# Kernel optimization log

Measured on AMD Instinct MI355X. Metric: run time of the kernel, lower is better.

## Reference

```python
import jax, jax.numpy as jnp
import numpy as np

MLP_DIMS = [256, 128, 64, 32, 1]

def setup_inputs() -> dict:
    key = jax.random.key(0)
    ks = jax.random.split(key, 16)
    N, C, sp = 2, 256, 512
    inp = {
        'points': jax.random.normal(ks[0], (N, C, sp), dtype=jnp.float32),
        'heatMap': jax.random.uniform(ks[1], (N, sp, sp), dtype=jnp.float32),
        'mask': jnp.ones((N, sp, sp), dtype=jnp.float32),
        'positiveMask': jax.random.uniform(ks[2], (N, sp, sp), dtype=jnp.float32),
    }
    # MLP params: 256->128->64->32->1, Kaiming-ish scale
    for i, (din, dout) in enumerate(zip(MLP_DIMS[:-1], MLP_DIMS[1:])):
        inp[f'W{i}'] = jax.random.normal(ks[4 + i], (din, dout), dtype=jnp.float32) * (1.0 / np.sqrt(din))
        inp[f'b{i}'] = jnp.zeros((dout,), dtype=jnp.float32)
    return inp


def _mlp(x, Ws, bs):
    # Linear+ReLU cascade; final layer is a raw logit (no activation).
    n = len(Ws)
    for i, (W, b) in enumerate(zip(Ws, bs)):
        x = jnp.einsum('...i,io->...o', x, W) + b
        if i < n - 1:
            x = jax.nn.relu(x)
    return x


def _bce_with_logits(logits, targets):
    # stable elementwise BCE-with-logits, reduction='none'
    return jnp.maximum(logits, 0.0) - logits * targets + jnp.log1p(jnp.exp(-jnp.abs(logits)))


def reference(points, heatMap, mask, positiveMask, W0, b0, W1, b1, W2, b2, W3, b3):
    p = jnp.transpose(points, (0, 2, 1))          # (N, sp, C)
    X = p[:, :, None, :] + p[:, None, :, :]       # (N, sp, sp, C)
    pred = _mlp(X, [W0, W1, W2, W3], [b0, b1, b2, b3])[..., 0]  # (N, sp, sp)
    loss = _bce_with_logits(pred, heatMap) * mask * positiveMask
    loss = loss.sum() / positiveMask.sum()
    return (pred, loss)
```

## Files before the change

### kernel.cpp

```cpp
#include <hip/hip_runtime.h>
#include <hip/hip_bf16.h>
#include <stdint.h>

#define N_ 2
#define C_ 256
#define SP 512
#define H1 128
#define H2 64
#define H3 32
#define NTILE 1056
#define GRID 256

using f32x4 = __attribute__((ext_vector_type(4))) float;
using u32x4 = __attribute__((ext_vector_type(4))) unsigned int;
using s16x8 = __attribute__((ext_vector_type(8))) short;

__device__ __forceinline__ uint32_t f2bf_rne(float x) {
    uint32_t u = __builtin_bit_cast(uint32_t, x);
    return (u + 0x7FFFu + ((u >> 16) & 1u)) >> 16;
}
__device__ __forceinline__ float bf2f(uint32_t h) {
    return __builtin_bit_cast(float, h << 16);
}
__device__ __forceinline__ uint32_t pkbf(float a, float b) {
    __hip_bfloat162 h = __float22bfloat162_rn(make_float2(a, b));
    uint32_t r;
    __builtin_memcpy(&r, &h, 4);
    return r;
}
__device__ __forceinline__ uint16_t bf1(float a) {
    __hip_bfloat16 h = __float2bfloat16(a);
    uint16_t r;
    __builtin_memcpy(&r, &h, 2);
    return r;
}
__device__ __forceinline__ f32x4 ntload4(const float* p) {
    return __builtin_nontemporal_load((const f32x4*)p);
}

__device__ __forceinline__ void unrank_tile(int tau, int& n, int& iBase, int& jBase)
{
    int nn = (tau >= 528) ? 1 : 0;
    int u = tau - nn * 528;
    int bi = (int)((65.0f - sqrtf(4225.0f - 8.0f * (float)u)) * 0.5f);
    int s = bi * (65 - bi) / 2;
    while (s > u) { --bi; s = bi * (65 - bi) / 2; }
    while (u - s >= 32 - bi) { ++bi; s = bi * (65 - bi) / 2; }
    int bj = bi + (u - s);
    n = nn; iBase = bi * 16; jBase = bj * 16;
}

__global__ __launch_bounds__(512) void k_precompA(
    const float* __restrict__ points, const float* __restrict__ W0,
    const float* __restrict__ b0,
    const float* __restrict__ W1, const float* __restrict__ W2,
    float* __restrict__ A,
    short* __restrict__ W1Th, short* __restrict__ W2Th, short* __restrict__ W2Tl,
    float* __restrict__ accum)
{
    int t = threadIdx.x;
    if (blockIdx.x == 0 && t < 4) accum[t] = 0.0f;
    int k4 = t & 31;
    int team = t >> 5;
    int rloc = team & 3, cq = team >> 2;
    int row = blockIdx.x * 4 + rloc;
    int n = row >> 9, i = row & (SP - 1);
    const float* pb = points + (size_t)n * C_ * SP + i;
    f32x4 p0 = {0.f, 0.f, 0.f, 0.f}, p1 = {0.f, 0.f, 0.f, 0.f};
    int c0 = cq * 64;
#pragma unroll 8
    for (int c = c0; c < c0 + 64; c += 2) {
        float s0 = pb[(size_t)c * SP];
        float s1 = pb[(size_t)(c + 1) * SP];
        f32x4 w0v = *(const f32x4*)(W0 + c * H1 + k4 * 4);
        f32x4 w1v = *(const f32x4*)(W0 + (c + 1) * H1 + k4 * 4);
#pragma unroll
        for (int e = 0; e < 4; ++e) {
            p0[e] = fmaf(s0, w0v[e], p0[e]);
            p1[e] = fmaf(s1, w1v[e], p1[e]);
        }
    }
#pragma unroll
    for (int e = 0; e < 4; ++e) p0[e] += p1[e];
    __shared__ f32x4 part[16][32];
    part[team][k4] = p0;
    __syncthreads();
    int r2 = t >> 7, kk = t & 127;
    float s = 0.5f * b0[kk]
            + part[r2][kk >> 2][kk & 3] + part[r2 + 4][kk >> 2][kk & 3]
            + part[r2 + 8][kk >> 2][kk & 3] + part[r2 + 12][kk >> 2][kk & 3];
    A[(size_t)(blockIdx.x * 4 + r2) * H1 + kk] = s;

    int gid = blockIdx.x * 512 + t;
    int gstride = gridDim.x * 512;
    for (int idx = gid; idx < H2 * H1; idx += gstride) {
        int col = idx >> 7, k = idx & 127;
        int sidx = col * 128 + ((((k >> 3) ^ (col & 15)) << 3) | (k & 7));
        W1Th[sidx] = (short)f2bf_rne(W1[k * H2 + col]);
    }
    for (int idx = gid; idx < H3 * H2; idx += gstride) {
        int col = idx >> 6, k = idx & 63;
        float wv = W2[k * H3 + col];
        uint32_t h = f2bf_rne(wv);
        int sidx = col * 64 + ((((k >> 3) ^ (col & 7)) << 3) | (k & 7));
        W2Th[sidx] = (short)h;
        W2Tl[sidx] = (short)f2bf_rne(wv - bf2f(h));
    }
}

__global__ __launch_bounds__(512, 2) void k_main(
    const float* __restrict__ A,
    const short* __restrict__ wtab,
    const float* __restrict__ b1, const float* __restrict__ b2,
    const float* __restrict__ W3, const float* __restrict__ b3,
    const float* __restrict__ heat, const float* __restrict__ mask,
    const float* __restrict__ pos,
    float* __restrict__ pred, float* __restrict__ accum, float* __restrict__ loss)
{
    __shared__ __align__(16) char smem[32768 + 32768 + 16384 + 2176 + 64];
    int t = threadIdx.x;
    int bid = blockIdx.x;
    int l = t & 63, w = t >> 6;
    int lc = l & 15, kg = l >> 4;
    char* x2b = smem + 32768 + w * 4096;
    char* x3b = smem + 65536 + w * 2048;
    char* zbB = smem + 81920;
    float* rb = (float*)(smem + 81920 + 2176);

    const short* lw1h = wtab;
    const short* lw2h = wtab + 8192;
    const short* lw2l = wtab + 10240;

    int rST = t >> 5, segST = t & 31;

    s16x8 bw3;
    {
        f32x4 wa = *(const f32x4*)(W3 + kg * 8);
        f32x4 wb = *(const f32x4*)(W3 + kg * 8 + 4);
        u32x4 wp;
        wp[0] = pkbf(wa[0], wa[1]);
        wp[1] = pkbf(wa[2], wa[3]);
        wp[2] = pkbf(wb[0], wb[1]);
        wp[3] = pkbf(wb[2], wb[3]);
        bw3 = __builtin_bit_cast(s16x8, wp);
    }
    float b3v = b3[0];

    float num = 0.0f, den = 0.0f;

    {
        int n0, ib0, jb0; unrank_tile(bid, n0, ib0, jb0);
        const float* Ab = A + (size_t)n0 * SP * H1;
        f32x4 va = ntload4(Ab + (size_t)(ib0 + rST) * H1 + segST * 4);
        f32x4 vb = ntload4(Ab + (size_t)(jb0 + rST) * H1 + segST * 4);
        *(f32x4*)(smem + rST * 512 + ((segST ^ rST) << 4)) = va;
        *(f32x4*)(smem + 8192 + rST * 512 + ((segST ^ rST) << 4)) = vb;
    }
    __syncthreads();

    int cur = 0, itp = 0;
    for (int tau = bid; tau < NTILE; tau += GRID, cur ^= 1, itp ^= 1) {
        int n, iBase, jBase; unrank_tile(tau, n, iBase, jBase);
        char* aiA = smem + cur * 16384;
        char* ajA = aiA + 8192;
        float* zb = (float*)(zbB + itp * 1088);

        bool hn = (tau + GRID < NTILE);
        f32x4 sva, svb;
        if (hn) {
            int n1, ib1, jb1; unrank_tile(tau + GRID, n1, ib1, jb1);
            const float* Ab1 = A + (size_t)n1 * SP * H1;
            sva = ntload4(Ab1 + (size_t)(ib1 + rST) * H1 + segST * 4);
            svb = ntload4(Ab1 + (size_t)(jb1 + rST) * H1 + segST * 4);
        }

        int pr = (t & 255) >> 4, pc = t & 15;
        size_t idx_e = (t < 256)
            ? ((size_t)n * SP + iBase + pr) * SP + (jBase + pc)
            : ((size_t)n * SP + jBase + pr) * SP + (iBase + pc);
        float tg_e = __builtin_nontemporal_load(heat + idx_e);
        float mk_e = __builtin_nontemporal_load(mask + idx_e);
        float pm_e = __builtin_nontemporal_load(pos + idx_e);

        f32x4 acc[2][4];
#pragma unroll
        for (int cf = 0; cf < 4; ++cf) {
            float bv = b1[cf * 16 + lc];
            acc[0][cf] = (f32x4){bv, bv, bv, bv};
            acc[1][cf] = (f32x4){bv, bv, bv, bv};
        }
#pragma unroll
        for (int ks = 0; ks < 4; ++ks) {
            int g0 = ks * 8 + kg * 2;
            f32x4 aj0 = *(const f32x4*)(ajA + lc * 512 + ((g0 ^ lc) << 4));
            f32x4 aj1 = *(const f32x4*)(ajA + lc * 512 + (((g0 + 1) ^ lc) << 4));
#pragma unroll
            for (int m = 0; m < 2; ++m) {
                int rl = 2 * w + m;
                f32x4 ai0 = *(const f32x4*)(aiA + rl * 512 + ((g0 ^ rl) << 4));
                f32x4 ai1 = *(const f32x4*)(aiA + rl * 512 + (((g0 + 1) ^ rl) << 4));
                float xs[8];
#pragma unroll
                for (int e = 0; e < 4; ++e) {
                    xs[e]     = fmaxf(ai0[e] + aj0[e], 0.0f);
                    xs[4 + e] = fmaxf(ai1[e] + aj1[e], 0.0f);
                }
                u32x4 hw;
#pragma unroll
                for (int p = 0; p < 4; ++p)
                    hw[p] = pkbf(xs[2 * p], xs[2 * p + 1]);
                s16x8 ahi = __builtin_bit_cast(s16x8, hw);
#pragma unroll
                for (int cf = 0; cf < 4; ++cf) {
                    int boff = (cf * 16 + lc) * 128 + (((ks * 4 + kg) ^ lc) << 3);
                    s16x8 bhi = *(const s16x8*)(lw1h + boff);
                    acc[m][cf] = __builtin_amdgcn_mfma_f32_16x16x32_bf16(ahi, bhi, acc[m][cf], 0, 0, 0);
                }
            }
        }

#pragma unroll
        for (int m = 0; m < 2; ++m) {
            char* x2 = x2b + m * 2048;
#pragma unroll
            for (int cf = 0; cf < 4; ++cf) {
                int g = cf * 2 + (lc >> 3);
#pragma unroll
                for (int r = 0; r < 4; ++r) {
                    int row = kg * 4 + r;
                    int off = row * 128 + ((g ^ (row & 7)) << 4) + (lc & 7) * 2;
                    *(uint16_t*)(x2 + off) = bf1(fmaxf(acc[m][cf][r], 0.0f));
                }
            }
        }
        f32x4 acc2[2][2];
#pragma unroll
        for (int cf = 0; cf < 2; ++cf) {
            float bv = b2[cf * 16 + lc];
            acc2[0][cf] = (f32x4){bv, bv, bv, bv};
            acc2[1][cf] = (f32x4){bv, bv, bv, bv};
        }
#pragma unroll
        for (int ks = 0; ks < 2; ++ks) {
#pragma unroll
            for (int m = 0; m < 2; ++m) {
                int aoff = lc * 128 + (((ks * 4 + kg) ^ (lc & 7)) << 4);
                s16x8 xa = *(const s16x8*)(x2b + m * 2048 + aoff);
#pragma unroll
                for (int cf = 0; cf < 2; ++cf) {
                    int b2off = (cf * 16 + lc) * 64 + (((ks * 4 + kg) ^ (lc & 7)) << 3);
                    s16x8 bh = *(const s16x8*)(lw2h + b2off);
                    s16x8 bl = *(const s16x8*)(lw2l + b2off);
                    acc2[m][cf] = __builtin_amdgcn_mfma_f32_16x16x32_bf16(xa, bh, acc2[m][cf], 0, 0, 0);
                    acc2[m][cf] = __builtin_amdgcn_mfma_f32_16x16x32_bf16(xa, bl, acc2[m][cf], 0, 0, 0);
                }
            }
        }
#pragma unroll
        for (int m = 0; m < 2; ++m) {
            char* x3 = x3b + m * 1024;
#pragma unroll
            for (int cf = 0; cf < 2; ++cf) {
                int g = cf * 2 + (lc >> 3);
#pragma unroll
                for (int r = 0; r < 4; ++r) {
                    int row = kg * 4 + r;
                    int off = row * 64 + ((g ^ (row & 3)) << 4) + (lc & 7) * 2;
                    *(uint16_t*)(x3 + off) = bf1(fmaxf(acc2[m][cf][r], 0.0f));
                }
            }
        }
#pragma unroll
        for (int m = 0; m < 2; ++m) {
            int a4off = lc * 64 + ((kg ^ (lc & 3)) << 4);
            s16x8 x4 = *(const s16x8*)(x3b + m * 1024 + a4off);
            f32x4 acc3 = (f32x4){b3v, b3v, b3v, b3v};
            acc3 = __builtin_amdgcn_mfma_f32_16x16x32_bf16(x4, bw3, acc3, 0, 0, 0);
            if (lc == 0) {
#pragma unroll
                for (int r = 0; r < 4; ++r)
                    zb[(2 * w + m) * 17 + kg * 4 + r] = acc3[r];
            }
        }

        if (hn) {
            char* Aalt = smem + (cur ^ 1) * 16384;
            *(f32x4*)(Aalt + rST * 512 + ((segST ^ rST) << 4)) = sva;
            *(f32x4*)(Aalt + 8192 + rST * 512 + ((segST ^ rST) << 4)) = svb;
        }
        __syncthreads();

        if (t < 256) {
            int i = iBase + pr, j = jBase + pc;
            if (j >= i) {
                float z = zb[pr * 17 + pc];
                __builtin_nontemporal_store(z, pred + idx_e);
                float bce = fmaxf(z, 0.0f) - z * tg_e + __logf(1.0f + __expf(-fabsf(z)));
                num += bce * mk_e * pm_e;
                den += pm_e;
            }
        } else {
            int J = jBase + pr, I = iBase + pc;
            if (J > I) {
                float z = zb[pc * 17 + pr];
                __builtin_nontemporal_store(z, pred + idx_e);
                float bce = fmaxf(z, 0.0f) - z * tg_e + __logf(1.0f + __expf(-fabsf(z)));
                num += bce * mk_e * pm_e;
                den += pm_e;
            }
        }
    }

#pragma unroll
    for (int off = 32; off > 0; off >>= 1) {
        num += __shfl_down(num, off, 64);
        den += __shfl_down(den, off, 64);
    }
    if (l == 0) { rb[w] = num; rb[8 + w] = den; }
    __syncthreads();
    if (t == 0) {
        float sn = 0.0f, sd = 0.0f;
#pragma unroll
        for (int q = 0; q < 8; ++q) { sn += rb[q]; sd += rb[8 + q]; }
        atomicAdd(&accum[0], sn);
        atomicAdd(&accum[1], sd);
        __threadfence();
        unsigned done = atomicAdd((unsigned*)&accum[2], 1u);
        if (done == GRID - 1) {
            float fn = atomicAdd(&accum[0], 0.0f);
            float fd = atomicAdd(&accum[1], 0.0f);
            loss[0] = fn / fd;
        }
    }
}

extern "C" void kernel_launch(void* const* d_in, const int* in_sizes, int n_in,
                              void* d_out, int out_size, void* d_ws, size_t ws_size,
                              hipStream_t stream)
{
    const float* points = (const float*)d_in[0];
    const float* heat   = (const float*)d_in[1];
    const float* mask   = (const float*)d_in[2];
    const float* pos    = (const float*)d_in[3];
    const float* W0     = (const float*)d_in[4];
    const float* b0     = (const float*)d_in[5];
    const float* W1     = (const float*)d_in[6];
    const float* b1     = (const float*)d_in[7];
    const float* W2     = (const float*)d_in[8];
    const float* b2     = (const float*)d_in[9];
    const float* W3     = (const float*)d_in[10];
    const float* b3     = (const float*)d_in[11];

    float* pred = (float*)d_out;
    float* loss = pred + (size_t)N_ * SP * SP;

    char* ws = (char*)d_ws;
    float* accum = (float*)ws;
    float* A     = (float*)(ws + 256);
    short* W1Th  = (short*)(ws + 256 + 524288);
    short* W2Th  = (short*)(ws + 256 + 524288 + 16384);
    short* W2Tl  = (short*)(ws + 256 + 524288 + 20480);

    k_precompA<<<256, 512, 0, stream>>>(points, W0, b0, W1, W2, A,
                                        W1Th, W2Th, W2Tl, accum);
    k_main<<<GRID, 512, 0, stream>>>(
        A, W1Th, b1, b2, W3, b3, heat, mask, pos, pred, accum, loss);
}
```

Measured before the change: 40.47 us.

## Compute first-layer projection with split-bf16 MFMA instead of scalar FMAs

The precompute kernel now computes A = points^T·W0 + b0/2 with 16x16x32 bf16 MFMA instructions. Each fp32 operand is split into a high and a low bf16 part, and three MFMAs (hi·lo, lo·hi, hi·hi) approximate fp32 accuracy. Each block handles 16 rows by 128 columns, so the grid shrinks from 256 blocks to 64 and the shared-memory partial-sum reduction is removed. The trade-off is a slightly different rounding and fewer blocks, which gives less parallelism for a kernel that is small to begin with.

```diff
diff --git a/kernel.cpp b/kernel.cpp
--- a/kernel.cpp
+++ b/kernel.cpp
@@ -33,6 +33,9 @@
     uint16_t r;
     __builtin_memcpy(&r, &h, 2);
     return r;
+}
+__device__ __forceinline__ uint32_t pack_hi2(uint32_t u0, uint32_t u1) {
+    return (u0 >> 16) | (u1 & 0xFFFF0000u);
 }
 __device__ __forceinline__ f32x4 ntload4(const float* p) {
     return __builtin_nontemporal_load((const f32x4*)p);
@@ -59,40 +62,63 @@
     float* __restrict__ accum)
 {
     int t = threadIdx.x;
-    if (blockIdx.x == 0 && t < 4) accum[t] = 0.0f;
-    int k4 = t & 31;
-    int team = t >> 5;
-    int rloc = team & 3, cq = team >> 2;
-    int row = blockIdx.x * 4 + rloc;
-    int n = row >> 9, i = row & (SP - 1);
-    const float* pb = points + (size_t)n * C_ * SP + i;
-    f32x4 p0 = {0.f, 0.f, 0.f, 0.f}, p1 = {0.f, 0.f, 0.f, 0.f};
-    int c0 = cq * 64;
-#pragma unroll 8
-    for (int c = c0; c < c0 + 64; c += 2) {
-        float s0 = pb[(size_t)c * SP];
-        float s1 = pb[(size_t)(c + 1) * SP];
-        f32x4 w0v = *(const f32x4*)(W0 + c * H1 + k4 * 4);
-        f32x4 w1v = *(const f32x4*)(W0 + (c + 1) * H1 + k4 * 4);
-#pragma unroll
-        for (int e = 0; e < 4; ++e) {
-            p0[e] = fmaf(s0, w0v[e], p0[e]);
-            p1[e] = fmaf(s1, w1v[e], p1[e]);
-        }
-    }
-#pragma unroll
-    for (int e = 0; e < 4; ++e) p0[e] += p1[e];
-    __shared__ f32x4 part[16][32];
-    part[team][k4] = p0;
-    __syncthreads();
-    int r2 = t >> 7, kk = t & 127;
-    float s = 0.5f * b0[kk]
-            + part[r2][kk >> 2][kk & 3] + part[r2 + 4][kk >> 2][kk & 3]
-            + part[r2 + 8][kk >> 2][kk & 3] + part[r2 + 12][kk >> 2][kk & 3];
-    A[(size_t)(blockIdx.x * 4 + r2) * H1 + kk] = s;
-
-    int gid = blockIdx.x * 512 + t;
-    int gstride = gridDim.x * 512;
+    int b = blockIdx.x;
+    if (b == 0 && t < 4) accum[t] = 0.0f;
+    int l = t & 63, w = t >> 6;
+    int lc = l & 15, kg = l >> 4;
+    int rBase = b * 16;
+    int n = rBase >> 9;
+    int iRow = (rBase & (SP - 1)) + lc;
+    const float* pb = points + (size_t)n * C_ * SP + iRow;
+    int hcol = w * 16 + lc;
+
+    f32x4 acc = {0.0f, 0.0f, 0.0f, 0.0f};
+#pragma unroll
+    for (int ks = 0; ks < 8; ++ks) {
+        int c0 = ks * 32 + kg * 8;
+        float xs[8];
+#pragma unroll
+        for (int e = 0; e < 8; ++e)
+            xs[e] = pb[(size_t)(c0 + e) * SP];
+        u32x4 ah, al;
+#pragma unroll
+        for (int p = 0; p < 4; ++p) {
+            uint32_t u0 = __builtin_bit_cast(uint32_t, xs[2 * p]);
+            uint32_t u1 = __builtin_bit_cast(uint32_t, xs[2 * p + 1]);
+            ah[p] = pack_hi2(u0, u1);
+            float l0 = xs[2 * p]     - bf2f(u0 >> 16);
+            float l1 = xs[2 * p + 1] - bf2f(u1 >> 16);
+            al[p] = pkbf(l0, l1);
+        }
+        s16x8 ahi = __builtin_bit_cast(s16x8, ah);
+        s16x8 alo = __builtin_bit_cast(s16x8, al);
+        float ws[8];
+#pragma unroll
+        for (int e = 0; e < 8; ++e)
+            ws[e] = W0[(size_t)(c0 + e) * H1 + hcol];
+        u32x4 bh, bl;
+#pragma unroll
+        for (int p = 0; p < 4; ++p) {
+            uint32_t u0 = __builtin_bit_cast(uint32_t, ws[2 * p]);
+            uint32_t u1 = __builtin_bit_cast(uint32_t, ws[2 * p + 1]);
+            bh[p] = pack_hi2(u0, u1);
+            float l0 = ws[2 * p]     - bf2f(u0 >> 16);
+            float l1 = ws[2 * p + 1] - bf2f(u1 >> 16);
+            bl[p] = pkbf(l0, l1);
+        }
+        s16x8 bhi = __builtin_bit_cast(s16x8, bh);
+        s16x8 blo = __builtin_bit_cast(s16x8, bl);
+        acc = __builtin_amdgcn_mfma_f32_16x16x32_bf16(ahi, blo, acc, 0, 0, 0);
+        acc = __builtin_amdgcn_mfma_f32_16x16x32_bf16(alo, bhi, acc, 0, 0, 0);
+        acc = __builtin_amdgcn_mfma_f32_16x16x32_bf16(ahi, bhi, acc, 0, 0, 0);
+    }
+    float bv = 0.5f * b0[hcol];
+#pragma unroll
+    for (int r = 0; r < 4; ++r)
+        A[(size_t)(rBase + kg * 4 + r) * H1 + hcol] = acc[r] + bv;
+
+    int gid = b * 512 + t;
+    int gstride = 64 * 512;
     for (int idx = gid; idx < H2 * H1; idx += gstride) {
         int col = idx >> 7, k = idx & 127;
         int sidx = col * 128 + ((((k >> 3) ^ (col & 15)) << 3) | (k & 7));
@@ -361,8 +387,8 @@
     short* W2Th  = (short*)(ws + 256 + 524288 + 16384);
     short* W2Tl  = (short*)(ws + 256 + 524288 + 20480);
 
-    k_precompA<<<256, 512, 0, stream>>>(points, W0, b0, W1, W2, A,
-                                        W1Th, W2Th, W2Tl, accum);
+    k_precompA<<<64, 512, 0, stream>>>(points, W0, b0, W1, W2, A,
+                                       W1Th, W2Th, W2Tl, accum);
     k_main<<<GRID, 512, 0, stream>>>(
         A, W1Th, b1, b2, W3, b3, heat, mask, pos, pred, accum, loss);
 }
```

After: 39.05 us, median of 2. -3.5%, faster.
